# Kernel tuning notes

Hardware: AMD Instinct MI355X
Metric: run time of the kernel (lower is better)

The kernel has to match this reference:

```python
import jax, jax.numpy as jnp
import numpy as np

B, T, H, L = 32, 256, 1024, 2
FORGET_BIAS = 1.0


def setup_inputs() -> dict:
    key = jax.random.key(0)
    k1, k2, k3, k4 = jax.random.split(key, 4)
    x = jax.random.normal(k1, (B, T, H), dtype=jnp.float32)
    lengths = jax.random.randint(k2, (B,), 1, T + 1, dtype=jnp.int32)
    Wx = jax.random.normal(k3, (L, H, 4 * H), dtype=jnp.float32) * 0.02
    Wh = jax.random.normal(k4, (L, H, 4 * H), dtype=jnp.float32) * 0.02
    b = jnp.zeros((L, 4 * H), dtype=jnp.float32)
    return {"x": x, "lengths": lengths, "Wx": Wx, "Wh": Wh, "b": b}


def _lstm_layer(x, lengths, Wx, Wh, b):
    """One TF-style LSTM layer over time with dynamic_rnn length masking.
    Gate order (i, j, f, o), forget_bias added to f. Returns (outputs, (h_T, c_T))."""
    Bb, Tt, _ = x.shape
    Hh = Wh.shape[0]
    # precompute input projections for all steps: [B, T, 4H]
    xproj = jnp.einsum('bti,ig->btg', x, Wx) + b

    def step(carry, inp):
        h, c = carry
        xt, t = inp  # xt: [B, 4H], t: scalar step index
        z = xt + h @ Wh  # [B, 4H]
        i, j, f, o = jnp.split(z, 4, axis=-1)
        c_new = jax.nn.sigmoid(f + FORGET_BIAS) * c + jax.nn.sigmoid(i) * jnp.tanh(j)
        h_new = jax.nn.sigmoid(o) * jnp.tanh(c_new)
        mask = (t < lengths)[:, None]  # [B,1]
        h2 = jnp.where(mask, h_new, h)
        c2 = jnp.where(mask, c_new, c)
        out = jnp.where(mask, h_new, 0.0)  # dynamic_rnn zeros outputs past length
        return (h2, c2), out

    init = (jnp.zeros((Bb, Hh), x.dtype), jnp.zeros((Bb, Hh), x.dtype))
    (hT, cT), outs = jax.lax.scan(step, init, (xproj.transpose(1, 0, 2), jnp.arange(Tt)))
    return outs.transpose(1, 0, 2), (hT, cT)


def reference(x, lengths, Wx, Wh, b):
    inp = x
    hs, cs = [], []
    for l in range(L):  # fixed small layer stack
        inp, (hT, cT) = _lstm_layer(inp, lengths, Wx[l], Wh[l], b[l])
        hs.append(hT)
        cs.append(cT)
    # rnnout: [B,T,H]; hidden: per-layer final (c,h) like TF LSTMStateTuple
    return inp, jnp.stack(cs), jnp.stack(hs)
```

## Files before the change

### kernel.cpp

```cpp
#include <hip/hip_runtime.h>

typedef unsigned short u16;
typedef unsigned int u32;
typedef unsigned long long u64;
typedef __attribute__((ext_vector_type(8))) short short8;
typedef __attribute__((ext_vector_type(4))) float f32x4;
typedef __attribute__((ext_vector_type(4))) u32 u32x4;
typedef __attribute__((ext_vector_type(2))) u32 u32x2;

#define RN_ 8388608
#define MFMA16(a, b, c) __builtin_amdgcn_mfma_f32_16x16x32_bf16(a, b, c, 0, 0, 0)

__device__ __forceinline__ u16 f2bf(float f) {
  union { float f; u32 u; } v; v.f = f;
  u32 r = v.u + 0x7fffu + ((v.u >> 16) & 1u);
  return (u16)(r >> 16);
}
__device__ __forceinline__ float bf2f(u16 h) {
  union { u32 u; float f; } v; v.u = ((u32)h) << 16;
  return v.f;
}
__device__ __forceinline__ u32 pk2(float a, float b) {
  return (u32)f2bf(a) | ((u32)f2bf(b) << 16);
}
__device__ __forceinline__ int permcol(int R) {
  return (R & 3) * 1024 + ((R >> 5) << 3) + ((R >> 2) & 7);
}
__device__ __forceinline__ float sigm(float x) { return 1.f / (1.f + __expf(-x)); }
__device__ __forceinline__ float tanh_(float x) {
  float e = __expf(2.f * x);
  return 1.f - 2.f / (e + 1.f);
}

__global__ __launch_bounds__(256) void transpose_convert(
    const float* __restrict__ Wx, const float* __restrict__ Wh,
    u16* __restrict__ WxT1, u16* __restrict__ WxT2,
    u16* __restrict__ WhT1, u16* __restrict__ WhT2) {
  __shared__ float lds[64][65];
  const int bid = blockIdx.x, tid = threadIdx.x;
  const int sel = bid >> 10;
  const int tile = bid & 1023;
  const int kt = tile & 15, rt = tile >> 4;
  const float* src;
  u16* dst;
  if (sel == 0)      { src = Wx;                       dst = WxT1; }
  else if (sel == 1) { src = Wx + (size_t)1024 * 4096; dst = WxT2; }
  else if (sel == 2) { src = Wh;                       dst = WhT1; }
  else               { src = Wh + (size_t)1024 * 4096; dst = WhT2; }
#pragma unroll
  for (int ii = 0; ii < 16; ++ii) {
    int idx = ii * 256 + tid;
    int r = idx >> 6, c = idx & 63;
    int run = c >> 3, u = c & 7;
    int blkLoc = run >> 2, gate = run & 3;
    int g = gate * 1024 + (rt * 2 + blkLoc) * 8 + u;
    lds[r][blkLoc * 32 + u * 4 + gate] = src[(size_t)(kt * 64 + r) * 4096 + g];
  }
  __syncthreads();
#pragma unroll
  for (int ii = 0; ii < 16; ++ii) {
    int idx = ii * 256 + tid;
    int rw = idx >> 6, cw = idx & 63;
    dst[(size_t)(rt * 64 + rw) * 1024 + kt * 64 + cw] = f2bf(lds[cw][rw]);
  }
}

template <int IS2>
__device__ void gemm_grp(char* smem, int gb,
    const float* __restrict__ Af32, const u16* __restrict__ Ahp,
    const u16* __restrict__ Bt, const float* __restrict__ bias,
    u16* __restrict__ Cring, const int* flags, int* gdone) {
  u16* As = (u16*)smem;
  u16* Bs = (u16*)(smem + 16384);
  const int tid = threadIdx.x;
  const int lane = tid & 63, w = tid >> 6;
  const int wm = w >> 1, wn = w & 1;
  const int l15 = lane & 15, lq = lane >> 4;
  const int srow = tid >> 2, qd = tid & 3;
  const int mg = gb >> 5, ng = gb & 31;
  const u32 rsw = (u32)((l15 & 7) << 4);

  for (int c = 0; c < 32; ++c) {
    if (w == 0) {
      const int thrA = IS2 ? 8 * (c + 1) : 8 * c - 24;
      const int thrB = 8 * c - 24;
      while (1) {
        bool ok = true;
        if (lane < 16) {
          u32x4 fv;
          const u32x4* fp = (const u32x4*)flags + lane;
          asm volatile("global_load_dwordx4 %0, %1, off sc0 sc1"
                       : "=v"(fv) : "v"(fp) : "memory");
          asm volatile("s_waitcnt vmcnt(0)" ::: "memory");
          __builtin_amdgcn_sched_barrier(0);
          ok = (int)fv[0] >= thrA && (int)fv[1] >= thrA &&
               (int)fv[2] >= thrA && (int)fv[3] >= thrA;
        } else if (IS2 && lane < 32) {
          u32x4 fv;
          const u32x4* fp = (const u32x4*)(flags + 64) + (lane - 16);
          asm volatile("global_load_dwordx4 %0, %1, off sc0 sc1"
                       : "=v"(fv) : "v"(fp) : "memory");
          asm volatile("s_waitcnt vmcnt(0)" ::: "memory");
          __builtin_amdgcn_sched_barrier(0);
          ok = (int)fv[0] >= thrB && (int)fv[1] >= thrB &&
               (int)fv[2] >= thrB && (int)fv[3] >= thrB;
        }
        if (__all(ok)) break;
        __builtin_amdgcn_s_sleep(8);
      }
    }
    __syncthreads();

    f32x4 acc[4][4];
#pragma unroll
    for (int i = 0; i < 4; ++i)
#pragma unroll
      for (int j = 0; j < 4; ++j) acc[i][j] = (f32x4){0.f, 0.f, 0.f, 0.f};

    for (int kt = 0; kt < 16; ++kt) {
      u32x4 aw[2][2], bv[2][2];
#pragma unroll
      for (int rr = 0; rr < 2; ++rr) {
        int row = rr * 64 + srow;
        const u32x4* bp = (const u32x4*)(Bt + (size_t)(ng * 128 + row) * 1024 + kt * 64 + qd * 16);
        bv[rr][0] = bp[0]; bv[rr][1] = bp[1];
        int rg = 256 * c + mg * 128 + row;
        if (IS2) {
          int tq = rg >> 5, b2 = rg & 31;
          int p = kt * 8 + qd * 2;
          const char* ap = (const char*)Ahp + (size_t)tq * 65536 +
                           (size_t)(p * 32 + b2) * 16;
          asm volatile("global_load_dwordx4 %0, %1, off sc0 sc1"
                       : "=v"(aw[rr][0]) : "v"(ap) : "memory");
          asm volatile("global_load_dwordx4 %0, %1, off sc0 sc1"
                       : "=v"(aw[rr][1]) : "v"(ap + 512) : "memory");
        } else {
          const f32x4* ap = (const f32x4*)(Af32 +
              ((size_t)(rg & 31) * 256 + (rg >> 5)) * 1024 + kt * 64 + qd * 16);
          f32x4 a0 = ap[0], a1 = ap[1], a2 = ap[2], a3 = ap[3];
          aw[rr][0][0] = pk2(a0[0], a0[1]); aw[rr][0][1] = pk2(a0[2], a0[3]);
          aw[rr][0][2] = pk2(a1[0], a1[1]); aw[rr][0][3] = pk2(a1[2], a1[3]);
          aw[rr][1][0] = pk2(a2[0], a2[1]); aw[rr][1][1] = pk2(a2[2], a2[3]);
          aw[rr][1][2] = pk2(a3[0], a3[1]); aw[rr][1][3] = pk2(a3[2], a3[3]);
        }
      }
      __syncthreads();
      if (IS2) {
        asm volatile("s_waitcnt vmcnt(0)" ::: "memory");
        __builtin_amdgcn_sched_barrier(0);
      }
#pragma unroll
      for (int rr = 0; rr < 2; ++rr) {
        int row = rr * 64 + srow;
        u32 sw = (u32)((row & 7) << 4);
        int base = row * 128 + qd * 32;
        *(u32x4*)((char*)As + ((base) ^ sw)) = aw[rr][0];
        *(u32x4*)((char*)As + ((base + 16) ^ sw)) = aw[rr][1];
        *(u32x4*)((char*)Bs + ((base) ^ sw)) = bv[rr][0];
        *(u32x4*)((char*)Bs + ((base + 16) ^ sw)) = bv[rr][1];
      }
      __syncthreads();
#pragma unroll
      for (int k2 = 0; k2 < 2; ++k2) {
        short8 af[4], bf[4];
#pragma unroll
        for (int f = 0; f < 4; ++f) {
          af[f] = *(const short8*)((const char*)As +
                   (((wm * 64 + f * 16 + l15) * 128 + k2 * 64 + lq * 16) ^ rsw));
          bf[f] = *(const short8*)((const char*)Bs +
                   (((wn * 64 + f * 16 + l15) * 128 + k2 * 64 + lq * 16) ^ rsw));
        }
#pragma unroll
        for (int fi = 0; fi < 4; ++fi)
#pragma unroll
          for (int fj = 0; fj < 4; ++fj)
            acc[fi][fj] = MFMA16(af[fi], bf[fj], acc[fi][fj]);
      }
    }
#pragma unroll
    for (int fj = 0; fj < 4; ++fj) {
      int gc = ng * 128 + wn * 64 + fj * 16 + l15;
      float bvv = bias[permcol(gc)];
#pragma unroll
      for (int fi = 0; fi < 4; ++fi) {
        int rr0 = (c & 3) * 256 + mg * 128 + wm * 64 + fi * 16 + lq * 4;
#pragma unroll
        for (int r = 0; r < 4; ++r) {
          u32 vv = (u32)f2bf(acc[fi][fj][r] + bvv);
          const u16* cp = Cring + (size_t)(rr0 + r) * 4096 + gc;
          asm volatile("global_store_short %0, %1, off sc0 sc1"
                       :: "v"(cp), "v"(vv) : "memory");
        }
      }
    }
    asm volatile("s_waitcnt vmcnt(0)" ::: "memory");
    __syncthreads();
    if (tid == 0)
      __hip_atomic_fetch_add(gdone + c, 1, __ATOMIC_RELAXED, __HIP_MEMORY_SCOPE_AGENT);
  }
}

#define ISSUE_FRAG(B, i_) do { \
  const int g_ = (i_) >> 2, j_ = (i_) & 3; \
  if (j_ == 0) asm volatile("global_load_dwordx4 %0, %1, off sc0 sc1" \
                            : "=v"(B[i_]) : "v"(pa[g_]) : "memory"); \
  else if (j_ == 1) asm volatile("global_load_dwordx4 %0, %1, off offset:256 sc0 sc1" \
                                 : "=v"(B[i_]) : "v"(pa[g_]) : "memory"); \
  else if (j_ == 2) asm volatile("global_load_dwordx4 %0, %1, off offset:2048 sc0 sc1" \
                                 : "=v"(B[i_]) : "v"(pa[g_]) : "memory"); \
  else asm volatile("global_load_dwordx4 %0, %1, off offset:2304 sc0 sc1" \
                    : "=v"(B[i_]) : "v"(pa[g_]) : "memory"); \
} while (0)
#define DRAIN0() do { asm volatile("s_waitcnt vmcnt(0)" ::: "memory"); \
  __builtin_amdgcn_sched_barrier(0); } while (0)
#define MFALL(B) do { _Pragma("unroll") for (int i_ = 0; i_ < 16; ++i_) { \
  const int ks_ = i_ >> 1, bc_ = i_ & 1; \
  acc[0][bc_] = MFMA16(afr[0][ks_], B[i_], acc[0][bc_]); \
  acc[1][bc_] = MFMA16(afr[1][ks_], B[i_], acc[1][bc_]); \
  acc[2][bc_] = MFMA16(afr[2][ks_], B[i_], acc[2][bc_]); \
  acc[3][bc_] = MFMA16(afr[3][ks_], B[i_], acc[3][bc_]); } } while (0)

template <int L>
__device__ void scan_grp(char* smem, int nb,
    const u16* __restrict__ xpring, const u16* __restrict__ Wt,
    const int* __restrict__ lengths, u64* hpub,
    int* flags_self, const int* gdone,
    float* __restrict__ outp, float* __restrict__ csf, float* __restrict__ hsf) {
  f32x4* partv = (f32x4*)smem;
  u16* h_stage = (u16*)(smem + 32768);
  float* out_stage = (float*)(smem + 33792);
  const int tid = threadIdx.x;
  const int lane = tid & 63, w = tid >> 6;
  const int l15 = lane & 15, q = lane >> 4;
  const int b = (w & 1) * 16 + l15;
  const int u0 = (w >> 1) * 4 + q;
  const int len = lengths[b];

  short8 afr[4][8];
#pragma unroll
  for (int tt = 0; tt < 4; ++tt)
#pragma unroll
    for (int ks = 0; ks < 8; ++ks)
      afr[tt][ks] = *(const short8*)(Wt + (size_t)(nb * 64 + tt * 16 + l15) * 1024 +
                                     w * 256 + ks * 32 + q * 8);

  f32x4 acc[4][2];
#pragma unroll
  for (int tt = 0; tt < 4; ++tt)
#pragma unroll
    for (int bc = 0; bc < 2; ++bc) acc[tt][bc] = (f32x4){0.f, 0.f, 0.f, 0.f};
  float c0 = 0.f, h0 = 0.f, c1 = 0.f, h1 = 0.f;

  const int lane_base = (w * 32 + q) * 512 + l15 * 16;

  for (int t = 0; t < 256; ++t) {
    if ((t & 7) == 0) {
      if (w == 0) {
        const int cidx = t >> 3;
        while (1) {
          bool ok = true;
          if (lane == 0) {
            u32 cd;
            asm volatile("global_load_dword %0, %1, off sc0 sc1"
                         : "=v"(cd) : "v"(gdone + cidx) : "memory");
            asm volatile("s_waitcnt vmcnt(0)" ::: "memory");
            __builtin_amdgcn_sched_barrier(0);
            ok = (int)cd >= 64;
          }
          if (__all(ok)) break;
          __builtin_amdgcn_s_sleep(2);
        }
      }
      __syncthreads();
    }

    const u16* xa = xpring + ((size_t)((t >> 3) & 3) * 256 + (t & 7) * 32 + b) * 4096 +
                    nb * 64 + u0 * 4;
    u32x2 xpv0, xpv1;
    asm volatile("global_load_dwordx2 %0, %1, off sc0 sc1"
                 : "=v"(xpv0) : "v"(xa) : "memory");
    asm volatile("global_load_dwordx2 %0, %1, off sc0 sc1"
                 : "=v"(xpv1) : "v"(xa + 32) : "memory");

    if (t > 0) {
      const char* hp = (const char*)hpub + (size_t)(t - 1) * 65536 + lane_base;
      const char* pa[4];
#pragma unroll
      for (int g = 0; g < 4; ++g) pa[g] = hp + g * 4096;
      __builtin_amdgcn_s_sleep(16);
      short8 bfv[16];
#pragma unroll
      for (int i = 0; i < 16; ++i) ISSUE_FRAG(bfv, i);
      u32 done = 0;
      while (1) {
        DRAIN0();
        {
#pragma unroll
          for (int i = 0; i < 16; ++i) {
            if (!(done & (1u << i))) {
              u32x4 vv = __builtin_bit_cast(u32x4, bfv[i]);
              bool ok = vv[0] != 0xFFFFFFFFu && vv[1] != 0xFFFFFFFFu &&
                        vv[2] != 0xFFFFFFFFu && vv[3] != 0xFFFFFFFFu;
              if (__all(ok)) done |= (1u << i);
            }
          }
        }
        if (done == 0xFFFFu) break;
#pragma unroll
        for (int i = 0; i < 16; ++i)
          if (!(done & (1u << i))) ISSUE_FRAG(bfv, i);
      }
      __builtin_amdgcn_sched_barrier(0);
      MFALL(bfv);
    } else {
      DRAIN0();
    }

#pragma unroll
    for (int tt = 0; tt < 4; ++tt)
#pragma unroll
      for (int bc = 0; bc < 2; ++bc) {
        partv[(w * 8 + tt * 2 + bc) * 64 + lane] = acc[tt][bc];
        acc[tt][bc] = (f32x4){0.f, 0.f, 0.f, 0.f};
      }
    __syncthreads();
    if ((t & 7) == 0 && t > 0 && tid == 0)
      __hip_atomic_store(flags_self + nb, t, __ATOMIC_RELAXED,
                         __HIP_MEMORY_SCOPE_AGENT);
    f32x4 s0 = (f32x4){0.f, 0.f, 0.f, 0.f};
    f32x4 s1 = (f32x4){0.f, 0.f, 0.f, 0.f};
#pragma unroll
    for (int w2 = 0; w2 < 4; ++w2) {
      s0 += partv[(w2 * 8 + w) * 64 + lane];
      s1 += partv[(w2 * 8 + 4 + w) * 64 + lane];
    }

    bool mk = t < len;
    {
      float zi = s0[0] + bf2f((u16)(xpv0[0] & 0xffffu));
      float zj = s0[1] + bf2f((u16)(xpv0[0] >> 16));
      float zf = s0[2] + bf2f((u16)(xpv0[1] & 0xffffu)) + 1.f;
      float zo = s0[3] + bf2f((u16)(xpv0[1] >> 16));
      float cn = sigm(zf) * c0 + sigm(zi) * tanh_(zj);
      float hn = sigm(zo) * tanh_(cn);
      c0 = mk ? cn : c0;
      h0 = mk ? hn : h0;
      float ov = mk ? hn : 0.f;
      h_stage[b * 16 + u0] = f2bf(ov);
      if (L) out_stage[b * 16 + u0] = ov;
    }
    {
      float zi = s1[0] + bf2f((u16)(xpv1[0] & 0xffffu));
      float zj = s1[1] + bf2f((u16)(xpv1[0] >> 16));
      float zf = s1[2] + bf2f((u16)(xpv1[1] & 0xffffu)) + 1.f;
      float zo = s1[3] + bf2f((u16)(xpv1[1] >> 16));
      float cn = sigm(zf) * c1 + sigm(zi) * tanh_(zj);
      float hn = sigm(zo) * tanh_(cn);
      c1 = mk ? cn : c1;
      h1 = mk ? hn : h1;
      float ov = mk ? hn : 0.f;
      h_stage[b * 16 + u0 + 8] = f2bf(ov);
      if (L) out_stage[b * 16 + u0 + 8] = ov;
    }
    __syncthreads();

    if (tid < 64) {
      int p = tid >> 5, bb = tid & 31;
      u32x4 pv = *(const u32x4*)((const char*)h_stage + bb * 32 + p * 16);
      char* hd = (char*)hpub + (size_t)t * 65536 +
                 (size_t)((nb * 2 + p) * 32 + bb) * 16;
      asm volatile("global_store_dwordx4 %0, %1, off sc0 sc1"
                   :: "v"(hd), "v"(pv) : "memory");
    }
    if (L && tid < 128) {
      int bb = tid >> 2, part = tid & 3;
      f32x4 ov = *(const f32x4*)(out_stage + bb * 16 + part * 4);
      *(f32x4*)(outp + ((size_t)bb * 256 + t) * 1024 + nb * 16 + part * 4) = ov;
    }
  }
  DRAIN0();
  __syncthreads();
  if (tid == 0)
    __hip_atomic_store(flags_self + nb, 256, __ATOMIC_RELAXED,
                       __HIP_MEMORY_SCOPE_AGENT);
  csf[L * 32768 + b * 1024 + nb * 16 + u0] = c0;
  csf[L * 32768 + b * 1024 + nb * 16 + u0 + 8] = c1;
  hsf[L * 32768 + b * 1024 + nb * 16 + u0] = h0;
  hsf[L * 32768 + b * 1024 + nb * 16 + u0 + 8] = h1;
}

__global__ __launch_bounds__(256, 1) void lstm_pipe(
    const float* __restrict__ x, const int* __restrict__ lengths,
    const float* __restrict__ bias,
    const u16* __restrict__ WxT1, const u16* __restrict__ WxT2,
    const u16* __restrict__ WhT1, const u16* __restrict__ WhT2,
    u16* xp1ring, u16* xp2ring,
    u64* hpub1, u64* hpub2, int* flags, float* outp) {
  __shared__ __align__(16) char smem[35840];
  int* g1done = flags + 128;
  int* g2done = flags + 160;
  const int bid = blockIdx.x;
  float* csf = outp + RN_;
  float* hsf = csf + 65536;
  if (bid < 64)
    gemm_grp<0>(smem, bid, x, nullptr, WxT1, bias, xp1ring, flags, g1done);
  else if (bid < 128)
    scan_grp<0>(smem, bid - 64, xp1ring, WhT1, lengths, hpub1, flags, g1done,
                outp, csf, hsf);
  else if (bid < 192)
    gemm_grp<1>(smem, bid - 128, nullptr, (const u16*)hpub1, WxT2, bias + 4096,
                xp2ring, flags, g2done);
  else
    scan_grp<1>(smem, bid - 192, xp2ring, WhT2, lengths, hpub2, flags + 64, g2done,
                outp, csf, hsf);
}

#define WS_WXT1 0u
#define WS_WXT2 (8u << 20)
#define WS_WHT1 (16u << 20)
#define WS_WHT2 (24u << 20)
#define WS_XP1 (32u << 20)
#define WS_XP2 (48u << 20)
#define WS_HPUB1 (64u << 20)
#define WS_HPUB2 (80u << 20)
#define WS_FLAGS (96u << 20)

extern "C" void kernel_launch(void* const* d_in, const int* in_sizes, int n_in,
                              void* d_out, int out_size, void* d_ws, size_t ws_size,
                              hipStream_t stream) {
  const float* x = (const float*)d_in[0];
  const int* lengths = (const int*)d_in[1];
  const float* Wx = (const float*)d_in[2];
  const float* Wh = (const float*)d_in[3];
  const float* bias = (const float*)d_in[4];
  float* outp = (float*)d_out;

  if (ws_size < (size_t)WS_FLAGS + 4096) return;

  char* ws = (char*)d_ws;
  u16* WxT1 = (u16*)(ws + WS_WXT1);
  u16* WxT2 = (u16*)(ws + WS_WXT2);
  u16* WhT1 = (u16*)(ws + WS_WHT1);
  u16* WhT2 = (u16*)(ws + WS_WHT2);
  u16* xp1ring = (u16*)(ws + WS_XP1);
  u16* xp2ring = (u16*)(ws + WS_XP2);
  u64* hpub1 = (u64*)(ws + WS_HPUB1);
  u64* hpub2 = (u64*)(ws + WS_HPUB2);
  int* flags = (int*)(ws + WS_FLAGS);

  hipMemsetAsync(flags, 0, 2048, stream);
  hipMemsetAsync(hpub1, 0xFF, 32u << 20, stream);
  transpose_convert<<<4096, 256, 0, stream>>>(Wx, Wh, WxT1, WxT2, WhT1, WhT2);
  lstm_pipe<<<256, 256, 0, stream>>>(x, lengths, bias, WxT1, WxT2, WhT1, WhT2,
                                     xp1ring, xp2ring, hpub1, hpub2, flags, outp);
}
```

Baseline: 1.089 ms.

## Halve scan workgroups to 32 per layer, each owning twice the hidden units

```diff
diff --git a/kernel.cpp b/kernel.cpp
--- a/kernel.cpp
+++ b/kernel.cpp
@@ -86,7 +86,7 @@
       const int thrB = 8 * c - 24;
       while (1) {
         bool ok = true;
-        if (lane < 16) {
+        if (lane < 8) {
           u32x4 fv;
           const u32x4* fp = (const u32x4*)flags + lane;
           asm volatile("global_load_dwordx4 %0, %1, off sc0 sc1"
@@ -95,9 +95,9 @@
           __builtin_amdgcn_sched_barrier(0);
           ok = (int)fv[0] >= thrA && (int)fv[1] >= thrA &&
                (int)fv[2] >= thrA && (int)fv[3] >= thrA;
-        } else if (IS2 && lane < 32) {
+        } else if (IS2 && lane < 16) {
           u32x4 fv;
-          const u32x4* fp = (const u32x4*)(flags + 64) + (lane - 16);
+          const u32x4* fp = (const u32x4*)(flags + 32) + (lane - 8);
           asm volatile("global_load_dwordx4 %0, %1, off sc0 sc1"
                        : "=v"(fv) : "v"(fp) : "memory");
           asm volatile("s_waitcnt vmcnt(0)" ::: "memory");
@@ -213,12 +213,6 @@
 } while (0)
 #define DRAIN0() do { asm volatile("s_waitcnt vmcnt(0)" ::: "memory"); \
   __builtin_amdgcn_sched_barrier(0); } while (0)
-#define MFALL(B) do { _Pragma("unroll") for (int i_ = 0; i_ < 16; ++i_) { \
-  const int ks_ = i_ >> 1, bc_ = i_ & 1; \
-  acc[0][bc_] = MFMA16(afr[0][ks_], B[i_], acc[0][bc_]); \
-  acc[1][bc_] = MFMA16(afr[1][ks_], B[i_], acc[1][bc_]); \
-  acc[2][bc_] = MFMA16(afr[2][ks_], B[i_], acc[2][bc_]); \
-  acc[3][bc_] = MFMA16(afr[3][ks_], B[i_], acc[3][bc_]); } } while (0)
 
 template <int L>
 __device__ void scan_grp(char* smem, int nb,
@@ -227,8 +221,8 @@
     int* flags_self, const int* gdone,
     float* __restrict__ outp, float* __restrict__ csf, float* __restrict__ hsf) {
   f32x4* partv = (f32x4*)smem;
-  u16* h_stage = (u16*)(smem + 32768);
-  float* out_stage = (float*)(smem + 33792);
+  u16* h_stage = (u16*)(smem + 65536);
+  float* out_stage = (float*)(smem + 67584);
   const int tid = threadIdx.x;
   const int lane = tid & 63, w = tid >> 6;
   const int l15 = lane & 15, q = lane >> 4;
@@ -236,20 +230,21 @@
   const int u0 = (w >> 1) * 4 + q;
   const int len = lengths[b];
 
-  short8 afr[4][8];
-#pragma unroll
-  for (int tt = 0; tt < 4; ++tt)
+  short8 afr[8][8];
+#pragma unroll
+  for (int tt = 0; tt < 8; ++tt)
 #pragma unroll
     for (int ks = 0; ks < 8; ++ks)
-      afr[tt][ks] = *(const short8*)(Wt + (size_t)(nb * 64 + tt * 16 + l15) * 1024 +
+      afr[tt][ks] = *(const short8*)(Wt + (size_t)(nb * 128 + tt * 16 + l15) * 1024 +
                                      w * 256 + ks * 32 + q * 8);
 
-  f32x4 acc[4][2];
-#pragma unroll
-  for (int tt = 0; tt < 4; ++tt)
+  f32x4 acc[8][2];
+#pragma unroll
+  for (int tt = 0; tt < 8; ++tt)
 #pragma unroll
     for (int bc = 0; bc < 2; ++bc) acc[tt][bc] = (f32x4){0.f, 0.f, 0.f, 0.f};
-  float c0 = 0.f, h0 = 0.f, c1 = 0.f, h1 = 0.f;
+  float cs[4] = {0.f, 0.f, 0.f, 0.f};
+  float hs[4] = {0.f, 0.f, 0.f, 0.f};
 
   const int lane_base = (w * 32 + q) * 512 + l15 * 16;
 
@@ -275,12 +270,12 @@
     }
 
     const u16* xa = xpring + ((size_t)((t >> 3) & 3) * 256 + (t & 7) * 32 + b) * 4096 +
-                    nb * 64 + u0 * 4;
-    u32x2 xpv0, xpv1;
-    asm volatile("global_load_dwordx2 %0, %1, off sc0 sc1"
-                 : "=v"(xpv0) : "v"(xa) : "memory");
-    asm volatile("global_load_dwordx2 %0, %1, off sc0 sc1"
-                 : "=v"(xpv1) : "v"(xa + 32) : "memory");
+                    nb * 128 + u0 * 4;
+    u32x2 xpv[4];
+#pragma unroll
+    for (int m = 0; m < 4; ++m)
+      asm volatile("global_load_dwordx2 %0, %1, off sc0 sc1"
+                   : "=v"(xpv[m]) : "v"(xa + m * 32) : "memory");
 
     if (t > 0) {
       const char* hp = (const char*)hpub + (size_t)(t - 1) * 65536 + lane_base;
@@ -311,71 +306,67 @@
           if (!(done & (1u << i))) ISSUE_FRAG(bfv, i);
       }
       __builtin_amdgcn_sched_barrier(0);
-      MFALL(bfv);
+#pragma unroll
+      for (int i = 0; i < 16; ++i) {
+        const int ks = i >> 1, bc = i & 1;
+#pragma unroll
+        for (int tt = 0; tt < 8; ++tt)
+          acc[tt][bc] = MFMA16(afr[tt][ks], bfv[i], acc[tt][bc]);
+      }
     } else {
       DRAIN0();
     }
 
 #pragma unroll
-    for (int tt = 0; tt < 4; ++tt)
+    for (int tt = 0; tt < 8; ++tt)
 #pragma unroll
       for (int bc = 0; bc < 2; ++bc) {
-        partv[(w * 8 + tt * 2 + bc) * 64 + lane] = acc[tt][bc];
+        partv[(w * 16 + tt * 2 + bc) * 64 + lane] = acc[tt][bc];
         acc[tt][bc] = (f32x4){0.f, 0.f, 0.f, 0.f};
       }
     __syncthreads();
     if ((t & 7) == 0 && t > 0 && tid == 0)
       __hip_atomic_store(flags_self + nb, t, __ATOMIC_RELAXED,
                          __HIP_MEMORY_SCOPE_AGENT);
-    f32x4 s0 = (f32x4){0.f, 0.f, 0.f, 0.f};
-    f32x4 s1 = (f32x4){0.f, 0.f, 0.f, 0.f};
-#pragma unroll
-    for (int w2 = 0; w2 < 4; ++w2) {
-      s0 += partv[(w2 * 8 + w) * 64 + lane];
-      s1 += partv[(w2 * 8 + 4 + w) * 64 + lane];
-    }
 
     bool mk = t < len;
-    {
-      float zi = s0[0] + bf2f((u16)(xpv0[0] & 0xffffu));
-      float zj = s0[1] + bf2f((u16)(xpv0[0] >> 16));
-      float zf = s0[2] + bf2f((u16)(xpv0[1] & 0xffffu)) + 1.f;
-      float zo = s0[3] + bf2f((u16)(xpv0[1] >> 16));
-      float cn = sigm(zf) * c0 + sigm(zi) * tanh_(zj);
+#pragma unroll
+    for (int m = 0; m < 4; ++m) {
+      const int tt = 2 * m + (w >> 1);
+      f32x4 s = (f32x4){0.f, 0.f, 0.f, 0.f};
+#pragma unroll
+      for (int w2 = 0; w2 < 4; ++w2)
+        s += partv[(w2 * 16 + tt * 2 + (w & 1)) * 64 + lane];
+      float zi = s[0] + bf2f((u16)(xpv[m][0] & 0xffffu));
+      float zj = s[1] + bf2f((u16)(xpv[m][0] >> 16));
+      float zf = s[2] + bf2f((u16)(xpv[m][1] & 0xffffu)) + 1.f;
+      float zo = s[3] + bf2f((u16)(xpv[m][1] >> 16));
+      float cn = sigm(zf) * cs[m] + sigm(zi) * tanh_(zj);
       float hn = sigm(zo) * tanh_(cn);
-      c0 = mk ? cn : c0;
-      h0 = mk ? hn : h0;
+      cs[m] = mk ? cn : cs[m];
+      hs[m] = mk ? hn : hs[m];
       float ov = mk ? hn : 0.f;
-      h_stage[b * 16 + u0] = f2bf(ov);
-      if (L) out_stage[b * 16 + u0] = ov;
-    }
-    {
-      float zi = s1[0] + bf2f((u16)(xpv1[0] & 0xffffu));
-      float zj = s1[1] + bf2f((u16)(xpv1[0] >> 16));
-      float zf = s1[2] + bf2f((u16)(xpv1[1] & 0xffffu)) + 1.f;
-      float zo = s1[3] + bf2f((u16)(xpv1[1] >> 16));
-      float cn = sigm(zf) * c1 + sigm(zi) * tanh_(zj);
-      float hn = sigm(zo) * tanh_(cn);
-      c1 = mk ? cn : c1;
-      h1 = mk ? hn : h1;
-      float ov = mk ? hn : 0.f;
-      h_stage[b * 16 + u0 + 8] = f2bf(ov);
-      if (L) out_stage[b * 16 + u0 + 8] = ov;
+      h_stage[b * 32 + u0 + 8 * m] = f2bf(ov);
+      if (L) out_stage[b * 32 + u0 + 8 * m] = ov;
     }
     __syncthreads();
 
     if (tid < 64) {
-      int p = tid >> 5, bb = tid & 31;
-      u32x4 pv = *(const u32x4*)((const char*)h_stage + bb * 32 + p * 16);
-      char* hd = (char*)hpub + (size_t)t * 65536 +
-                 (size_t)((nb * 2 + p) * 32 + bb) * 16;
-      asm volatile("global_store_dwordx4 %0, %1, off sc0 sc1"
-                   :: "v"(hd), "v"(pv) : "memory");
-    }
-    if (L && tid < 128) {
-      int bb = tid >> 2, part = tid & 3;
-      f32x4 ov = *(const f32x4*)(out_stage + bb * 16 + part * 4);
-      *(f32x4*)(outp + ((size_t)bb * 256 + t) * 1024 + nb * 16 + part * 4) = ov;
+#pragma unroll
+      for (int g = 0; g < 2; ++g) {
+        int gi = tid * 2 + g;
+        int p = gi >> 5, bb = gi & 31;
+        u32x4 pv = *(const u32x4*)((const char*)h_stage + bb * 64 + p * 16);
+        char* hd = (char*)hpub + (size_t)t * 65536 +
+                   (size_t)((nb * 4 + p) * 32 + bb) * 16;
+        asm volatile("global_store_dwordx4 %0, %1, off sc0 sc1"
+                     :: "v"(hd), "v"(pv) : "memory");
+      }
+    }
+    if (L) {
+      int bb = tid >> 3, part = tid & 7;
+      f32x4 ov = *(const f32x4*)(out_stage + bb * 32 + part * 4);
+      *(f32x4*)(outp + ((size_t)bb * 256 + t) * 1024 + nb * 32 + part * 4) = ov;
     }
   }
   DRAIN0();
@@ -383,10 +374,11 @@
   if (tid == 0)
     __hip_atomic_store(flags_self + nb, 256, __ATOMIC_RELAXED,
                        __HIP_MEMORY_SCOPE_AGENT);
-  csf[L * 32768 + b * 1024 + nb * 16 + u0] = c0;
-  csf[L * 32768 + b * 1024 + nb * 16 + u0 + 8] = c1;
-  hsf[L * 32768 + b * 1024 + nb * 16 + u0] = h0;
-  hsf[L * 32768 + b * 1024 + nb * 16 + u0 + 8] = h1;
+#pragma unroll
+  for (int m = 0; m < 4; ++m) {
+    csf[L * 32768 + b * 1024 + nb * 32 + u0 + 8 * m] = cs[m];
+    hsf[L * 32768 + b * 1024 + nb * 32 + u0 + 8 * m] = hs[m];
+  }
 }
 
 __global__ __launch_bounds__(256, 1) void lstm_pipe(
@@ -396,22 +388,22 @@
     const u16* __restrict__ WhT1, const u16* __restrict__ WhT2,
     u16* xp1ring, u16* xp2ring,
     u64* hpub1, u64* hpub2, int* flags, float* outp) {
-  __shared__ __align__(16) char smem[35840];
-  int* g1done = flags + 128;
-  int* g2done = flags + 160;
+  __shared__ __align__(16) char smem[71680];
+  int* g1done = flags + 64;
+  int* g2done = flags + 96;
   const int bid = blockIdx.x;
   float* csf = outp + RN_;
   float* hsf = csf + 65536;
   if (bid < 64)
     gemm_grp<0>(smem, bid, x, nullptr, WxT1, bias, xp1ring, flags, g1done);
-  else if (bid < 128)
+  else if (bid < 96)
     scan_grp<0>(smem, bid - 64, xp1ring, WhT1, lengths, hpub1, flags, g1done,
                 outp, csf, hsf);
-  else if (bid < 192)
-    gemm_grp<1>(smem, bid - 128, nullptr, (const u16*)hpub1, WxT2, bias + 4096,
+  else if (bid < 160)
+    gemm_grp<1>(smem, bid - 96, nullptr, (const u16*)hpub1, WxT2, bias + 4096,
                 xp2ring, flags, g2done);
   else
-    scan_grp<1>(smem, bid - 192, xp2ring, WhT2, lengths, hpub2, flags + 64, g2done,
+    scan_grp<1>(smem, bid - 160, xp2ring, WhT2, lengths, hpub2, flags + 32, g2done,
                 outp, csf, hsf);
 }
 
@@ -451,6 +443,6 @@
   hipMemsetAsync(flags, 0, 2048, stream);
   hipMemsetAsync(hpub1, 0xFF, 32u << 20, stream);
   transpose_convert<<<4096, 256, 0, stream>>>(Wx, Wh, WxT1, WxT2, WhT1, WhT2);
-  lstm_pipe<<<256, 256, 0, stream>>>(x, lengths, bias, WxT1, WxT2, WhT1, WhT2,
+  lstm_pipe<<<192, 256, 0, stream>>>(x, lengths, bias, WxT1, WxT2, WhT1, WhT2,
                                      xp1ring, xp2ring, hpub1, hpub2, flags, outp);
 }
```

Measured after the change: 1.582 ms. 45.3% more time.
